# Optimization experiments

Hardware: AMD Instinct MI355X
Metric: run time of the kernel (lower is better)

## Reference

```python
import jax, jax.numpy as jnp
import numpy as np

DMODEL = 1024
DHIDDEN = 1024
N_HEAD = 16
HEAD_DIM = DHIDDEN // N_HEAD
B, S = 4, 2048


def setup_inputs() -> dict:
    key = jax.random.key(0)
    ks = jax.random.split(key, 10)
    sc = 1.0 / np.sqrt(DMODEL)
    return {
        "x": jax.random.normal(ks[0], (B, S, DMODEL), dtype=jnp.float32),
        "Wq": jax.random.normal(ks[1], (DMODEL, DHIDDEN), dtype=jnp.float32) * sc,
        "bq": jnp.zeros((DHIDDEN,), dtype=jnp.float32),
        "Wk": jax.random.normal(ks[2], (DMODEL, DHIDDEN), dtype=jnp.float32) * sc,
        "bk": jnp.zeros((DHIDDEN,), dtype=jnp.float32),
        "Wv": jax.random.normal(ks[3], (DMODEL, DHIDDEN), dtype=jnp.float32) * sc,
        "bv": jnp.zeros((DHIDDEN,), dtype=jnp.float32),
        "Wo": jax.random.normal(ks[4], (DHIDDEN, DMODEL), dtype=jnp.float32) * sc,
        "bo": jnp.zeros((DMODEL,), dtype=jnp.float32),
        "ln_gamma": jnp.ones((DMODEL,), dtype=jnp.float32),
        "ln_beta": jnp.zeros((DMODEL,), dtype=jnp.float32),
    }


def _layernorm(x, gamma, beta, eps=1e-5):
    mu = jnp.mean(x, axis=-1, keepdims=True)
    var = jnp.var(x, axis=-1, keepdims=True)
    return (x - mu) * jax.lax.rsqrt(var + eps) * gamma + beta


def reference(x, Wq, bq, Wk, bk, Wv, bv, Wo, bo, ln_gamma, ln_beta):
    b, s, _ = x.shape
    h = _layernorm(x, ln_gamma, ln_beta)           # [B,S,D]
    q = h @ Wq + bq                                 # [B,S,Dh]
    k = h @ Wk + bk
    v = h @ Wv + bv
    # [B,H,S,hd]
    q = q.reshape(b, s, N_HEAD, HEAD_DIM).transpose(0, 2, 1, 3)
    k = k.reshape(b, s, N_HEAD, HEAD_DIM).transpose(0, 2, 1, 3)
    v = v.reshape(b, s, N_HEAD, HEAD_DIM).transpose(0, 2, 1, 3)
    scores = jnp.einsum("bhqd,bhkd->bhqk", q, k) / np.sqrt(HEAD_DIM)
    causal = jnp.tril(jnp.ones((s, s), dtype=bool))  # [S,S]
    scores = jnp.where(causal, scores, jnp.finfo(scores.dtype).min)
    attn = jax.nn.softmax(scores, axis=-1)           # [B,H,S,S]
    out = jnp.einsum("bhqk,bhkd->bhqd", attn, v)     # [B,H,S,hd]
    out = out.transpose(0, 2, 1, 3).reshape(b, s, DHIDDEN)
    return out @ Wo + bo
```

## Files before the change

kernel.cpp:

```cpp
#include <hip/hip_runtime.h>


typedef short short8 __attribute__((ext_vector_type(8)));
typedef float floatx4 __attribute__((ext_vector_type(4)));
typedef unsigned short ushort4v __attribute__((ext_vector_type(4)));
typedef unsigned int uint2v __attribute__((ext_vector_type(2)));

#define MFMA16(a, b, c) __builtin_amdgcn_mfma_f32_16x16x32_bf16((a), (b), (c), 0, 0, 0)

__device__ __forceinline__ unsigned short f2bf(float f) {
  unsigned int u = __float_as_uint(f);
  u += 0x7FFFu + ((u >> 16) & 1u);
  return (unsigned short)(u >> 16);
}

#if defined(__has_builtin)
#if __has_builtin(__builtin_amdgcn_cvt_pk_bf16_f32)
#define HAVE_PK_BF16 1
#endif
#if __has_builtin(__builtin_amdgcn_exp2f)
#define EXP2(x) __builtin_amdgcn_exp2f(x)
#endif
#if __has_builtin(__builtin_amdgcn_rcpf)
#define RCP(x) __builtin_amdgcn_rcpf(x)
#endif
#endif
#ifndef EXP2
#define EXP2(x) exp2f(x)
#endif
#ifndef RCP
#define RCP(x) (1.0f / (x))
#endif

__device__ __forceinline__ unsigned int pk_bf16(float a, float b) {
#ifdef HAVE_PK_BF16
  typedef __bf16 bf16x2_t __attribute__((ext_vector_type(2)));
  union { bf16x2_t v; unsigned int u; } cvt;
  cvt.v = __builtin_amdgcn_cvt_pk_bf16_f32(a, b);
  return cvt.u;
#else
  return (unsigned int)f2bf(a) | ((unsigned int)f2bf(b) << 16);
#endif
}

__device__ __forceinline__ void async_lds16(const void* g, void* l) {
  __builtin_amdgcn_global_load_lds(
      (const __attribute__((address_space(1))) void*)g,
      (__attribute__((address_space(3))) void*)l, 16, 0, 0);
}

__global__ __launch_bounds__(256) void prep_kernel(
    const float* __restrict__ wq, const float* __restrict__ wk,
    const float* __restrict__ wv, const float* __restrict__ wo,
    unsigned short* __restrict__ wqkvT, unsigned short* __restrict__ woT,
    const float* __restrict__ x, const float* __restrict__ gamma,
    const float* __restrict__ beta, unsigned short* __restrict__ h) {
  __shared__ float t[64][65];
  __shared__ float sm[4], qm[4];
  const int id = (int)blockIdx.x;
  const int tid = threadIdx.x;
  if (id < 1024) {
    const int mz = id >> 8, rem = id & 255;
    const int n0 = (rem & 15) * 64, k0 = (rem >> 4) * 64;
    const int r = tid >> 6, c = tid & 63;
    const float* src = (mz == 0) ? wq : (mz == 1) ? wk : (mz == 2) ? wv : wo;
    unsigned short* dst = (mz == 3) ? woT : (wqkvT + (size_t)mz * 1024 * 1024);
#pragma unroll
    for (int i = r; i < 64; i += 4) t[i][c] = src[(size_t)(k0 + i) * 1024 + n0 + c];
    __syncthreads();
#pragma unroll
    for (int i = r; i < 64; i += 4)
      dst[(size_t)(n0 + i) * 1024 + k0 + c] = f2bf(t[c][i]);
    return;
  }
  const int row = id - 1024;
  const float4 xv = ((const float4*)(x + (size_t)row * 1024))[tid];
  float s = xv.x + xv.y + xv.z + xv.w;
  float q = xv.x * xv.x + xv.y * xv.y + xv.z * xv.z + xv.w * xv.w;
#pragma unroll
  for (int off = 32; off > 0; off >>= 1) {
    s += __shfl_xor(s, off, 64);
    q += __shfl_xor(q, off, 64);
  }
  const int wave = tid >> 6, lane = tid & 63;
  if (lane == 0) { sm[wave] = s; qm[wave] = q; }
  __syncthreads();
  s = sm[0] + sm[1] + sm[2] + sm[3];
  q = qm[0] + qm[1] + qm[2] + qm[3];
  const float mean = s * (1.0f / 1024.0f);
  const float var = q * (1.0f / 1024.0f) - mean * mean;
  const float rstd = rsqrtf(var + 1e-5f);
  const float4 g = ((const float4*)gamma)[tid];
  const float4 bb = ((const float4*)beta)[tid];
  ushort4v o;
  o.x = f2bf((xv.x - mean) * rstd * g.x + bb.x);
  o.y = f2bf((xv.y - mean) * rstd * g.y + bb.y);
  o.z = f2bf((xv.z - mean) * rstd * g.z + bb.z);
  o.w = f2bf((xv.w - mean) * rstd * g.w + bb.w);
  ((ushort4v*)(h + (size_t)row * 1024))[tid] = o;
}

#define GEMM128_MAIN(A_, Bt_, m0_, n0_)                                         \
  __shared__ __align__(16) unsigned short lA[128 * 64];                         \
  __shared__ __align__(16) unsigned short lB[128 * 64];                         \
  const int tid = threadIdx.x;                                                  \
  const int wave = tid >> 6, lane = tid & 63, quad = lane >> 4, l15 = lane & 15;\
  const int wm = wave >> 1, wn = wave & 1;                                      \
  const int m0 = (m0_), n0 = (n0_);                                             \
  const int srow = tid >> 3, schunk = tid & 7;                                  \
  const int swz = l15 & 7;                                                      \
  floatx4 acc[4][4];                                                            \
  _Pragma("unroll") for (int i = 0; i < 4; i++)                                 \
  _Pragma("unroll") for (int j = 0; j < 4; j++)                                 \
      acc[i][j] = (floatx4){0.f, 0.f, 0.f, 0.f};                                \
  for (int kt = 0; kt < 16; kt++) {                                             \
    const int k0 = kt * 64;                                                     \
    __syncthreads();                                                            \
    _Pragma("unroll") for (int j = 0; j < 4; j++) {                             \
      const int row_ = j * 32 + srow;                                           \
      const int gch_ = schunk ^ (row_ & 7);                                     \
      async_lds16(A_ + (size_t)(m0 + row_) * 1024 + k0 + gch_ * 8,              \
                  (char*)lA + j * 4096 + wave * 1024);                          \
      async_lds16(Bt_ + (size_t)(n0 + row_) * 1024 + k0 + gch_ * 8,             \
                  (char*)lB + j * 4096 + wave * 1024);                          \
    }                                                                           \
    __syncthreads();                                                            \
    _Pragma("unroll") for (int kk = 0; kk < 2; kk++) {                          \
      const int ch = (kk * 4 + quad) ^ swz;                                     \
      short8 af[4], bf[4];                                                      \
      _Pragma("unroll") for (int i = 0; i < 4; i++) {                           \
        af[i] = *(const short8*)(lA + (wm * 64 + i * 16 + l15) * 64 + ch * 8);  \
        bf[i] = *(const short8*)(lB + (wn * 64 + i * 16 + l15) * 64 + ch * 8);  \
      }                                                                         \
      _Pragma("unroll") for (int mt = 0; mt < 4; mt++)                          \
      _Pragma("unroll") for (int nt = 0; nt < 4; nt++)                          \
          acc[mt][nt] = MFMA16(af[mt], bf[nt], acc[mt][nt]);                    \
    }                                                                           \
  }

__global__ __launch_bounds__(512, 2) void gemm_qkv(
    const unsigned short* __restrict__ A, const unsigned short* __restrict__ Bt,
    const float* __restrict__ bq, const float* __restrict__ bk,
    const float* __restrict__ bv, unsigned short* __restrict__ qo,
    unsigned short* __restrict__ ko, unsigned short* __restrict__ vT) {
  __shared__ __align__(16) unsigned short lA[2][2][128 * 64];
  __shared__ __align__(16) unsigned short lB[2][2][128 * 64];
  const int tid = threadIdx.x;
  const int wave = tid >> 6, lane = tid & 63, quad = lane >> 4, l15 = lane & 15;
  const int wm = wave >> 2, wn = wave & 3;
  const int id = (int)blockIdx.x;
  const int xcd = id & 7, rr = id >> 3;
  const int m0 = (xcd * 4 + (rr & 3)) * 256;
  const int n0 = (rr >> 2) * 256;

  const int srow8 = tid >> 3, chunk8 = tid & 7;
  const int gch = chunk8 ^ (srow8 & 7);
  const int wave1024 = wave * 1024;
  const int swz = l15 & 7;
  const int ch0 = quad ^ swz, ch1 = (4 + quad) ^ swz;

  const unsigned short* pA0 = A + (size_t)(m0 + srow8) * 1024 + gch * 8;
  const unsigned short* pA1 = pA0 + (size_t)128 * 1024;
  const unsigned short* pB0 = Bt + (size_t)(n0 + srow8) * 1024 + gch * 8;
  const unsigned short* pB1 = pB0 + (size_t)128 * 1024;

  const unsigned short* rdA[2] = {&lA[0][wm][0] + l15 * 64,
                                  &lA[1][wm][0] + l15 * 64};
  const unsigned short* rdB[2] = {&lB[0][wn >> 1][0] + ((wn & 1) * 64 + l15) * 64,
                                  &lB[1][wn >> 1][0] + ((wn & 1) * 64 + l15) * 64};

  floatx4 acc[8][4];
#pragma unroll
  for (int i = 0; i < 8; i++)
#pragma unroll
    for (int j = 0; j < 4; j++) acc[i][j] = (floatx4){0.f, 0.f, 0.f, 0.f};

  short8 bF[4][2], aQ0[2][2], aQ1[2][2], aQ2[2][2], aQ3[2][2];

#define STG(p_, k0_, dst_)                                                     \
  {                                                                            \
    _Pragma("unroll") for (int j_ = 0; j_ < 2; j_++)                           \
        async_lds16((p_) + (size_t)j_ * 65536 + (k0_),                         \
                    (char*)(dst_) + j_ * 8192 + wave1024);                     \
  }
#define LDB(buf_)                                                              \
  _Pragma("unroll") for (int n_ = 0; n_ < 4; n_++) {                           \
    bF[n_][0] = *(const short8*)(rdB[buf_] + n_ * 1024 + ch0 * 8);             \
    bF[n_][1] = *(const short8*)(rdB[buf_] + n_ * 1024 + ch1 * 8);             \
  }
#define LDA(dst_, mb_, buf_)                                                   \
  _Pragma("unroll") for (int mm_ = 0; mm_ < 2; mm_++) {                        \
    dst_[mm_][0] = *(const short8*)(rdA[buf_] + ((mb_) + mm_) * 1024 + ch0 * 8);\
    dst_[mm_][1] = *(const short8*)(rdA[buf_] + ((mb_) + mm_) * 1024 + ch1 * 8);\
  }
#define MFQ(af_, q_)                                                           \
  __builtin_amdgcn_s_setprio(1);                                              \
  _Pragma("unroll") for (int mm_ = 0; mm_ < 2; mm_++)                          \
  _Pragma("unroll") for (int n_ = 0; n_ < 4; n_++) {                           \
    acc[(q_)*2 + mm_][n_] = MFMA16(af_[mm_][0], bF[n_][0], acc[(q_)*2 + mm_][n_]); \
    acc[(q_)*2 + mm_][n_] = MFMA16(af_[mm_][1], bF[n_][1], acc[(q_)*2 + mm_][n_]); \
  }                                                                            \
  __builtin_amdgcn_s_setprio(0);
#define BAR()                                                                  \
  {                                                                            \
    asm volatile("" ::: "memory");                                             \
    __builtin_amdgcn_s_barrier();                                              \
    asm volatile("" ::: "memory");                                             \
  }
#define WAITV(n_)                                                              \
  {                                                                            \
    asm volatile("s_waitcnt vmcnt(" #n_ ")" ::: "memory");                     \
    __builtin_amdgcn_sched_barrier(0);                                         \
  }

  STG(pB0, 0, &lB[0][0][0]);
  STG(pB1, 0, &lB[0][1][0]);
  STG(pA0, 0, &lA[0][0][0]);
  STG(pA1, 0, &lA[0][1][0]);
  STG(pB0, 64, &lB[1][0][0]);
  STG(pB1, 64, &lB[1][1][0]);
  STG(pA0, 64, &lA[1][0][0]);
  WAITV(6);
  BAR();

  for (int i = 0; i < 7; i++) {
    const int kA = (2 * i + 1) * 64;
    const int kB = kA + 64;
    const int kC = kB + 64;
    LDB(0); LDA(aQ0, 0, 0);
    STG(pA1, kA, &lA[1][1][0]);
    BAR(); MFQ(aQ0, 0); BAR();
    LDA(aQ1, 2, 0); LDA(aQ2, 4, 0);
    STG(pB0, kB, &lB[0][0][0]);
    BAR(); MFQ(aQ1, 1); BAR();
    LDA(aQ3, 6, 0);
    STG(pB1, kB, &lB[0][1][0]);
    BAR(); MFQ(aQ2, 2); BAR();
    STG(pA0, kB, &lA[0][0][0]);
    WAITV(6);
    BAR(); MFQ(aQ3, 3); BAR();
    LDB(1); LDA(aQ0, 0, 1);
    STG(pA1, kB, &lA[0][1][0]);
    BAR(); MFQ(aQ0, 0); BAR();
    LDA(aQ1, 2, 1); LDA(aQ2, 4, 1);
    STG(pB0, kC, &lB[1][0][0]);
    BAR(); MFQ(aQ1, 1); BAR();
    LDA(aQ3, 6, 1);
    STG(pB1, kC, &lB[1][1][0]);
    BAR(); MFQ(aQ2, 2); BAR();
    STG(pA0, kC, &lA[1][0][0]);
    WAITV(6);
    BAR(); MFQ(aQ3, 3); BAR();
  }
  LDB(0); LDA(aQ0, 0, 0);
  STG(pA1, 15 * 64, &lA[1][1][0]);
  BAR(); MFQ(aQ0, 0); BAR();
  LDA(aQ1, 2, 0); LDA(aQ2, 4, 0);
  BAR(); MFQ(aQ1, 1); BAR();
  LDA(aQ3, 6, 0);
  BAR(); MFQ(aQ2, 2); BAR();
  WAITV(0);
  BAR(); MFQ(aQ3, 3); BAR();
  LDB(1); LDA(aQ0, 0, 1);
  MFQ(aQ0, 0);
  LDA(aQ1, 2, 1); LDA(aQ2, 4, 1);
  MFQ(aQ1, 1);
  LDA(aQ3, 6, 1);
  MFQ(aQ2, 2);
  MFQ(aQ3, 3);

  const int sel = n0 >> 10;
  const float* bias = (sel == 0) ? bq : (sel == 1) ? bk : bv;
  const float oscale = (sel == 0) ? 0.18033688011112042f : 1.0f;
#pragma unroll
  for (int nt = 0; nt < 4; nt++) {
    const int n = n0 + wn * 64 + nt * 16 + l15;
    const int nn = n & 1023;
    const float bia = bias[nn];
    const int hidx = nn >> 6, d = nn & 63;
#pragma unroll
    for (int mt = 0; mt < 8; mt++) {
      const int mb = m0 + wm * 128 + mt * 16 + quad * 4;
      const int b = mb >> 11, sdx = mb & 2047;
      if (sel == 2) {
        ushort4v pk;
#pragma unroll
        for (int r = 0; r < 4; r++) pk[r] = f2bf(acc[mt][nt][r] + bia);
        *(ushort4v*)(vT + ((size_t)(b * 16 + hidx) * 64 + d) * 2048 + sdx) = pk;
      } else {
        unsigned short* dst =
            ((sel == 0) ? qo : ko) + ((size_t)(b * 16 + hidx) * 2048 + sdx) * 64 + d;
#pragma unroll
        for (int r = 0; r < 4; r++)
          dst[(size_t)r * 64] = f2bf((acc[mt][nt][r] + bia) * oscale);
      }
    }
  }
#undef STG
#undef LDB
#undef LDA
#undef MFQ
#undef BAR
#undef WAITV
}

__global__ __launch_bounds__(256) void gemm_out(
    const unsigned short* __restrict__ A, const unsigned short* __restrict__ Bt,
    const float* __restrict__ bo, float* __restrict__ out) {
  const int id = (int)blockIdx.x;
  GEMM128_MAIN(A, Bt, (id >> 3) * 128, (id & 7) * 128)
#pragma unroll
  for (int nt = 0; nt < 4; nt++) {
    const int n = n0 + wn * 64 + nt * 16 + l15;
    const float bia = bo[n];
#pragma unroll
    for (int mt = 0; mt < 4; mt++) {
      const int m = m0 + wm * 64 + mt * 16 + quad * 4;
#pragma unroll
      for (int r = 0; r < 4; r++) out[(size_t)(m + r) * 1024 + n] = acc[mt][nt][r] + bia;
    }
  }
}

__global__ __launch_bounds__(256, 4) void attn_kernel(
    const unsigned short* __restrict__ q, const unsigned short* __restrict__ k,
    const unsigned short* __restrict__ vT, unsigned short* __restrict__ ao) {
  __shared__ __align__(16) unsigned short lK[2][64 * 64];
  __shared__ __align__(16) unsigned short lV[2][64 * 64];
  __shared__ __align__(16) unsigned short lP[4][16 * 64];
  const int tid = threadIdx.x;
  const int wave = tid >> 6, lane = tid & 63, quad = lane >> 4, l15 = lane & 15;
  const int id = (int)blockIdx.x;
  const int bh = (id & 7) * 8 + ((id >> 3) & 7);
  const int qx = id >> 6;
  const int b = bh >> 4, hh = bh & 15;
  const int qtA = 31 - qx, qtB = qx;
  const int q0wA = qtA * 64 + wave * 16, q0wB = qtB * 64 + wave * 16;
  const int ntiles = qtA + 1;

  const unsigned short* qb = q + (size_t)bh * 2048 * 64;
  const unsigned short* kb = k + (size_t)bh * 2048 * 64;
  const unsigned short* vb = vT + (size_t)bh * 64 * 2048;
  unsigned short* pw = &lP[wave][0];

  const int srow = tid >> 3, schunk = tid & 7;

  const short8 ones8 = {0x3F80, 0x3F80, 0x3F80, 0x3F80,
                        0x3F80, 0x3F80, 0x3F80, 0x3F80};

  const int sw = l15 & 7;
  const int ph0 = (0 * 4 + quad) ^ sw, ph1 = (1 * 4 + quad) ^ sw;

#define STAGE_TILE(src_, rstride_, cbase_, dst_)                                 \
  _Pragma("unroll") for (int j = 0; j < 2; j++) {                                \
    const int row_ = j * 32 + srow;                                              \
    const int gch_ = schunk ^ (row_ & 7);                                        \
    async_lds16(src_ + (size_t)row_ * (rstride_) + (cbase_) + gch_ * 8,          \
                (char*)(dst_) + j * 4096 + wave * 1024);                         \
  }

  short8 qfA[2], qfB[2];
#pragma unroll
  for (int hf = 0; hf < 2; hf++) {
    qfA[hf] = *(const short8*)(qb + (size_t)(q0wA + l15) * 64 + hf * 32 + quad * 8);
    qfB[hf] = *(const short8*)(qb + (size_t)(q0wB + l15) * 64 + hf * 32 + quad * 8);
  }

  floatx4 oA[4], oB[4];
#pragma unroll
  for (int nt = 0; nt < 4; nt++) {
    oA[nt] = (floatx4){0.f, 0.f, 0.f, 0.f};
    oB[nt] = (floatx4){0.f, 0.f, 0.f, 0.f};
  }
  floatx4 laccA = {0.f, 0.f, 0.f, 0.f}, laccB = {0.f, 0.f, 0.f, 0.f};

  STAGE_TILE(kb, 64, 0, &lK[0][0])
  STAGE_TILE(vb, 2048, 0, &lV[0][0])
  int kbase = 0;
  for (int t = 0; t < ntiles; t++, kbase += 64) {
    __syncthreads();
    if (t + 1 < ntiles) {
      const int nb = (t + 1) & 1;
      STAGE_TILE(kb, 64, (size_t)(kbase + 64) * 64, &lK[nb][0])
      STAGE_TILE(vb, 2048, (size_t)(kbase + 64), &lV[nb][0])
    }
    const unsigned short* lKc = &lK[t & 1][0];
    const unsigned short* lVc = &lV[t & 1][0];
    const bool dual = (t <= qtB);

    floatx4 scA[4], scB[4];
#pragma unroll
    for (int nt = 0; nt < 4; nt++) {
      scA[nt] = (floatx4){0.f, 0.f, 0.f, 0.f};
      scB[nt] = (floatx4){0.f, 0.f, 0.f, 0.f};
      const short8 kf0 = *(const short8*)(lKc + (nt * 16 + l15) * 64 + ph0 * 8);
      const short8 kf1 = *(const short8*)(lKc + (nt * 16 + l15) * 64 + ph1 * 8);
      scA[nt] = MFMA16(kf0, qfA[0], scA[nt]);
      scA[nt] = MFMA16(kf1, qfA[1], scA[nt]);
      if (dual) {
        scB[nt] = MFMA16(kf0, qfB[0], scB[nt]);
        scB[nt] = MFMA16(kf1, qfB[1], scB[nt]);
      }
    }

    {
      const bool needmask = (kbase + 63 > q0wA);
      const int qg = q0wA + l15;
#pragma unroll
      for (int nt = 0; nt < 4; nt++) {
        float p0 = EXP2(scA[nt][0]), p1 = EXP2(scA[nt][1]);
        float p2 = EXP2(scA[nt][2]), p3 = EXP2(scA[nt][3]);
        if (needmask) {
          const int kk = kbase + nt * 16 + quad * 4;
          if (kk + 0 > qg) p0 = 0.f;
          if (kk + 1 > qg) p1 = 0.f;
          if (kk + 2 > qg) p2 = 0.f;
          if (kk + 3 > qg) p3 = 0.f;
        }
        uint2v pk2;
        pk2.x = pk_bf16(p0, p1);
        pk2.y = pk_bf16(p2, p3);
        const int phys = (nt * 2 + (quad >> 1)) ^ sw;
        *(uint2v*)(pw + l15 * 64 + phys * 8 + (quad & 1) * 4) = pk2;
      }
    }
    asm volatile("s_waitcnt lgkmcnt(0)" ::: "memory");
    short8 pfA0 = *(const short8*)(pw + l15 * 64 + ph0 * 8);
    short8 pfA1 = *(const short8*)(pw + l15 * 64 + ph1 * 8);

    short8 pfB0, pfB1;
    if (dual) {
      const bool needmask = (kbase + 63 > q0wB);
      const int qg = q0wB + l15;
#pragma unroll
      for (int nt = 0; nt < 4; nt++) {
        float p0 = EXP2(scB[nt][0]), p1 = EXP2(scB[nt][1]);
        float p2 = EXP2(scB[nt][2]), p3 = EXP2(scB[nt][3]);
        if (needmask) {
          const int kk = kbase + nt * 16 + quad * 4;
          if (kk + 0 > qg) p0 = 0.f;
          if (kk + 1 > qg) p1 = 0.f;
          if (kk + 2 > qg) p2 = 0.f;
          if (kk + 3 > qg) p3 = 0.f;
        }
        uint2v pk2;
        pk2.x = pk_bf16(p0, p1);
        pk2.y = pk_bf16(p2, p3);
        const int phys = (nt * 2 + (quad >> 1)) ^ sw;
        *(uint2v*)(pw + l15 * 64 + phys * 8 + (quad & 1) * 4) = pk2;
      }
      asm volatile("s_waitcnt lgkmcnt(0)" ::: "memory");
      pfB0 = *(const short8*)(pw + l15 * 64 + ph0 * 8);
      pfB1 = *(const short8*)(pw + l15 * 64 + ph1 * 8);
    }

#pragma unroll
    for (int hf = 0; hf < 2; hf++) {
      const short8 pfA = hf ? pfA1 : pfA0;
      laccA = MFMA16(ones8, pfA, laccA);
      if (dual) laccB = MFMA16(ones8, hf ? pfB1 : pfB0, laccB);
      const int ph = hf ? ph1 : ph0;
#pragma unroll
      for (int nt = 0; nt < 4; nt++) {
        const short8 vf = *(const short8*)(lVc + (nt * 16 + l15) * 64 + ph * 8);
        oA[nt] = MFMA16(vf, pfA, oA[nt]);
        if (dual) oB[nt] = MFMA16(vf, hf ? pfB1 : pfB0, oB[nt]);
      }
    }
  }

  {
    const float linv = RCP(laccA[0]);
    unsigned short* dst = ao + ((size_t)b * 2048 + q0wA + l15) * 1024 + hh * 64;
#pragma unroll
    for (int nt = 0; nt < 4; nt++) {
      uint2v pk2;
      pk2.x = pk_bf16(oA[nt][0] * linv, oA[nt][1] * linv);
      pk2.y = pk_bf16(oA[nt][2] * linv, oA[nt][3] * linv);
      *(uint2v*)(dst + nt * 16 + quad * 4) = pk2;
    }
  }
  {
    const float linv = RCP(laccB[0]);
    unsigned short* dst = ao + ((size_t)b * 2048 + q0wB + l15) * 1024 + hh * 64;
#pragma unroll
    for (int nt = 0; nt < 4; nt++) {
      uint2v pk2;
      pk2.x = pk_bf16(oB[nt][0] * linv, oB[nt][1] * linv);
      pk2.y = pk_bf16(oB[nt][2] * linv, oB[nt][3] * linv);
      *(uint2v*)(dst + nt * 16 + quad * 4) = pk2;
    }
  }
#undef STAGE_TILE
}

extern "C" void kernel_launch(void* const* d_in, const int* in_sizes, int n_in,
                              void* d_out, int out_size, void* d_ws, size_t ws_size,
                              hipStream_t stream) {
  const float* x = (const float*)d_in[0];
  const float* Wq = (const float*)d_in[1];
  const float* bq = (const float*)d_in[2];
  const float* Wk = (const float*)d_in[3];
  const float* bk = (const float*)d_in[4];
  const float* Wv = (const float*)d_in[5];
  const float* bv = (const float*)d_in[6];
  const float* Wo = (const float*)d_in[7];
  const float* bo = (const float*)d_in[8];
  const float* gamma = (const float*)d_in[9];
  const float* beta = (const float*)d_in[10];
  float* out = (float*)d_out;

  char* ws = (char*)d_ws;
  unsigned short* wqkvT = (unsigned short*)(ws + 0);
  unsigned short* woT   = (unsigned short*)(ws + 6291456);
  unsigned short* h     = (unsigned short*)(ws + 8388608);
  unsigned short* qb    = (unsigned short*)(ws + 25165824);
  unsigned short* kb    = (unsigned short*)(ws + 41943040);
  unsigned short* vT    = (unsigned short*)(ws + 58720256);
  unsigned short* ao    = (unsigned short*)(ws + 75497472);

  hipLaunchKernelGGL(prep_kernel, dim3(9216), dim3(256), 0, stream,
                     Wq, Wk, Wv, Wo, wqkvT, woT, x, gamma, beta, h);
  hipLaunchKernelGGL(gemm_qkv, dim3(384), dim3(512), 0, stream,
                     h, wqkvT, bq, bk, bv, qb, kb, vT);
  hipLaunchKernelGGL(attn_kernel, dim3(1024), dim3(256), 0, stream, qb, kb, vT, ao);
  hipLaunchKernelGGL(gemm_out, dim3(512), dim3(256), 0, stream, ao, woT, bo, out);
}
```

Baseline: 276.5 us.

## Replace hand-pipelined 256x256 QKV GEMM with 128x128 tiles and LDS-staged epilogue

Result: faster. 262.1 us (-5.2%).

```diff
diff --git a/kernel.cpp b/kernel.cpp
--- a/kernel.cpp
+++ b/kernel.cpp
@@ -101,8 +101,9 @@
 }
 
 #define GEMM128_MAIN(A_, Bt_, m0_, n0_)                                         \
-  __shared__ __align__(16) unsigned short lA[128 * 64];                         \
-  __shared__ __align__(16) unsigned short lB[128 * 64];                         \
+  __shared__ __align__(16) unsigned short lAB[2][128 * 64];                     \
+  unsigned short* const lA = &lAB[0][0];                                        \
+  unsigned short* const lB = &lAB[1][0];                                        \
   const int tid = threadIdx.x;                                                  \
   const int wave = tid >> 6, lane = tid & 63, quad = lane >> 4, l15 = lane & 15;\
   const int wm = wave >> 1, wn = wave & 1;                                      \
@@ -138,170 +139,75 @@
     }                                                                           \
   }
 
-__global__ __launch_bounds__(512, 2) void gemm_qkv(
+__global__ __launch_bounds__(256) void gemm_qkv(
     const unsigned short* __restrict__ A, const unsigned short* __restrict__ Bt,
     const float* __restrict__ bq, const float* __restrict__ bk,
     const float* __restrict__ bv, unsigned short* __restrict__ qo,
     unsigned short* __restrict__ ko, unsigned short* __restrict__ vT) {
-  __shared__ __align__(16) unsigned short lA[2][2][128 * 64];
-  __shared__ __align__(16) unsigned short lB[2][2][128 * 64];
-  const int tid = threadIdx.x;
-  const int wave = tid >> 6, lane = tid & 63, quad = lane >> 4, l15 = lane & 15;
-  const int wm = wave >> 2, wn = wave & 3;
   const int id = (int)blockIdx.x;
   const int xcd = id & 7, rr = id >> 3;
-  const int m0 = (xcd * 4 + (rr & 3)) * 256;
-  const int n0 = (rr >> 2) * 256;
-
-  const int srow8 = tid >> 3, chunk8 = tid & 7;
-  const int gch = chunk8 ^ (srow8 & 7);
-  const int wave1024 = wave * 1024;
-  const int swz = l15 & 7;
-  const int ch0 = quad ^ swz, ch1 = (4 + quad) ^ swz;
-
-  const unsigned short* pA0 = A + (size_t)(m0 + srow8) * 1024 + gch * 8;
-  const unsigned short* pA1 = pA0 + (size_t)128 * 1024;
-  const unsigned short* pB0 = Bt + (size_t)(n0 + srow8) * 1024 + gch * 8;
-  const unsigned short* pB1 = pB0 + (size_t)128 * 1024;
-
-  const unsigned short* rdA[2] = {&lA[0][wm][0] + l15 * 64,
-                                  &lA[1][wm][0] + l15 * 64};
-  const unsigned short* rdB[2] = {&lB[0][wn >> 1][0] + ((wn & 1) * 64 + l15) * 64,
-                                  &lB[1][wn >> 1][0] + ((wn & 1) * 64 + l15) * 64};
-
-  floatx4 acc[8][4];
-#pragma unroll
-  for (int i = 0; i < 8; i++)
-#pragma unroll
-    for (int j = 0; j < 4; j++) acc[i][j] = (floatx4){0.f, 0.f, 0.f, 0.f};
-
-  short8 bF[4][2], aQ0[2][2], aQ1[2][2], aQ2[2][2], aQ3[2][2];
-
-#define STG(p_, k0_, dst_)                                                     \
-  {                                                                            \
-    _Pragma("unroll") for (int j_ = 0; j_ < 2; j_++)                           \
-        async_lds16((p_) + (size_t)j_ * 65536 + (k0_),                         \
-                    (char*)(dst_) + j_ * 8192 + wave1024);                     \
-  }
-#define LDB(buf_)                                                              \
-  _Pragma("unroll") for (int n_ = 0; n_ < 4; n_++) {                           \
-    bF[n_][0] = *(const short8*)(rdB[buf_] + n_ * 1024 + ch0 * 8);             \
-    bF[n_][1] = *(const short8*)(rdB[buf_] + n_ * 1024 + ch1 * 8);             \
-  }
-#define LDA(dst_, mb_, buf_)                                                   \
-  _Pragma("unroll") for (int mm_ = 0; mm_ < 2; mm_++) {                        \
-    dst_[mm_][0] = *(const short8*)(rdA[buf_] + ((mb_) + mm_) * 1024 + ch0 * 8);\
-    dst_[mm_][1] = *(const short8*)(rdA[buf_] + ((mb_) + mm_) * 1024 + ch1 * 8);\
-  }
-#define MFQ(af_, q_)                                                           \
-  __builtin_amdgcn_s_setprio(1);                                              \
-  _Pragma("unroll") for (int mm_ = 0; mm_ < 2; mm_++)                          \
-  _Pragma("unroll") for (int n_ = 0; n_ < 4; n_++) {                           \
-    acc[(q_)*2 + mm_][n_] = MFMA16(af_[mm_][0], bF[n_][0], acc[(q_)*2 + mm_][n_]); \
-    acc[(q_)*2 + mm_][n_] = MFMA16(af_[mm_][1], bF[n_][1], acc[(q_)*2 + mm_][n_]); \
-  }                                                                            \
-  __builtin_amdgcn_s_setprio(0);
-#define BAR()                                                                  \
-  {                                                                            \
-    asm volatile("" ::: "memory");                                             \
-    __builtin_amdgcn_s_barrier();                                              \
-    asm volatile("" ::: "memory");                                             \
-  }
-#define WAITV(n_)                                                              \
-  {                                                                            \
-    asm volatile("s_waitcnt vmcnt(" #n_ ")" ::: "memory");                     \
-    __builtin_amdgcn_sched_barrier(0);                                         \
-  }
-
-  STG(pB0, 0, &lB[0][0][0]);
-  STG(pB1, 0, &lB[0][1][0]);
-  STG(pA0, 0, &lA[0][0][0]);
-  STG(pA1, 0, &lA[0][1][0]);
-  STG(pB0, 64, &lB[1][0][0]);
-  STG(pB1, 64, &lB[1][1][0]);
-  STG(pA0, 64, &lA[1][0][0]);
-  WAITV(6);
-  BAR();
-
-  for (int i = 0; i < 7; i++) {
-    const int kA = (2 * i + 1) * 64;
-    const int kB = kA + 64;
-    const int kC = kB + 64;
-    LDB(0); LDA(aQ0, 0, 0);
-    STG(pA1, kA, &lA[1][1][0]);
-    BAR(); MFQ(aQ0, 0); BAR();
-    LDA(aQ1, 2, 0); LDA(aQ2, 4, 0);
-    STG(pB0, kB, &lB[0][0][0]);
-    BAR(); MFQ(aQ1, 1); BAR();
-    LDA(aQ3, 6, 0);
-    STG(pB1, kB, &lB[0][1][0]);
-    BAR(); MFQ(aQ2, 2); BAR();
-    STG(pA0, kB, &lA[0][0][0]);
-    WAITV(6);
-    BAR(); MFQ(aQ3, 3); BAR();
-    LDB(1); LDA(aQ0, 0, 1);
-    STG(pA1, kB, &lA[0][1][0]);
-    BAR(); MFQ(aQ0, 0); BAR();
-    LDA(aQ1, 2, 1); LDA(aQ2, 4, 1);
-    STG(pB0, kC, &lB[1][0][0]);
-    BAR(); MFQ(aQ1, 1); BAR();
-    LDA(aQ3, 6, 1);
-    STG(pB1, kC, &lB[1][1][0]);
-    BAR(); MFQ(aQ2, 2); BAR();
-    STG(pA0, kC, &lA[1][0][0]);
-    WAITV(6);
-    BAR(); MFQ(aQ3, 3); BAR();
-  }
-  LDB(0); LDA(aQ0, 0, 0);
-  STG(pA1, 15 * 64, &lA[1][1][0]);
-  BAR(); MFQ(aQ0, 0); BAR();
-  LDA(aQ1, 2, 0); LDA(aQ2, 4, 0);
-  BAR(); MFQ(aQ1, 1); BAR();
-  LDA(aQ3, 6, 0);
-  BAR(); MFQ(aQ2, 2); BAR();
-  WAITV(0);
-  BAR(); MFQ(aQ3, 3); BAR();
-  LDB(1); LDA(aQ0, 0, 1);
-  MFQ(aQ0, 0);
-  LDA(aQ1, 2, 1); LDA(aQ2, 4, 1);
-  MFQ(aQ1, 1);
-  LDA(aQ3, 6, 1);
-  MFQ(aQ2, 2);
-  MFQ(aQ3, 3);
-
+  GEMM128_MAIN(A, Bt, (rr / 3) * 128, (xcd * 3 + (rr % 3)) * 128)
   const int sel = n0 >> 10;
   const float* bias = (sel == 0) ? bq : (sel == 1) ? bk : bv;
   const float oscale = (sel == 0) ? 0.18033688011112042f : 1.0f;
-#pragma unroll
-  for (int nt = 0; nt < 4; nt++) {
-    const int n = n0 + wn * 64 + nt * 16 + l15;
-    const int nn = n & 1023;
-    const float bia = bias[nn];
-    const int hidx = nn >> 6, d = nn & 63;
-#pragma unroll
-    for (int mt = 0; mt < 8; mt++) {
-      const int mb = m0 + wm * 128 + mt * 16 + quad * 4;
-      const int b = mb >> 11, sdx = mb & 2047;
-      if (sel == 2) {
+  unsigned short* const st = &lAB[0][0];
+  const int b16 = (m0 >> 11) * 16;
+  const int h0 = (n0 & 1023) >> 6;
+  const int ms = m0 & 2047;
+  __syncthreads();
+  if (sel == 2) {
+#pragma unroll
+    for (int nt = 0; nt < 4; nt++) {
+      const int nl = wn * 64 + nt * 16 + l15;
+      const float bia = bias[(n0 + nl) & 1023];
+      const int x = (nl & 15) << 1;
+#pragma unroll
+      for (int mt = 0; mt < 4; mt++) {
+        const int chunk = wm * 16 + mt * 4 + quad;
         ushort4v pk;
 #pragma unroll
         for (int r = 0; r < 4; r++) pk[r] = f2bf(acc[mt][nt][r] + bia);
-        *(ushort4v*)(vT + ((size_t)(b * 16 + hidx) * 64 + d) * 2048 + sdx) = pk;
-      } else {
-        unsigned short* dst =
-            ((sel == 0) ? qo : ko) + ((size_t)(b * 16 + hidx) * 2048 + sdx) * 64 + d;
-#pragma unroll
-        for (int r = 0; r < 4; r++)
-          dst[(size_t)r * 64] = f2bf((acc[mt][nt][r] + bia) * oscale);
-      }
-    }
-  }
-#undef STG
-#undef LDB
-#undef LDA
-#undef MFQ
-#undef BAR
-#undef WAITV
+        *(ushort4v*)((char*)st + nl * 256 + ((chunk ^ x) << 3)) = pk;
+      }
+    }
+    __syncthreads();
+#pragma unroll
+    for (int p = 0; p < 8; p++) {
+      const int nl = p * 16 + (tid >> 4);
+      const int j2 = tid & 15;
+      const short8 vv =
+          *(const short8*)((char*)st + nl * 256 + ((j2 ^ (nl & 15)) << 4));
+      *(short8*)(vT + ((size_t)(b16 + h0 + (nl >> 6)) * 64 + (nl & 63)) * 2048 +
+                 ms + j2 * 8) = vv;
+    }
+  } else {
+#pragma unroll
+    for (int nt = 0; nt < 4; nt++) {
+      const int nl = wn * 64 + nt * 16 + l15;
+      const float bia = bias[(n0 + nl) & 1023];
+      const int chunk = nl >> 3, nin = nl & 7;
+#pragma unroll
+      for (int mt = 0; mt < 4; mt++) {
+#pragma unroll
+        for (int r = 0; r < 4; r++) {
+          const int ml = wm * 64 + mt * 16 + quad * 4 + r;
+          *(unsigned short*)((char*)st + ml * 256 + ((chunk ^ (ml & 7)) << 4) +
+                             nin * 2) = f2bf((acc[mt][nt][r] + bia) * oscale);
+        }
+      }
+    }
+    __syncthreads();
+    unsigned short* const dq = (sel == 0) ? qo : ko;
+#pragma unroll
+    for (int p = 0; p < 8; p++) {
+      const int ml = p * 16 + (tid >> 4);
+      const int j = tid & 15;
+      const short8 vv =
+          *(const short8*)((char*)st + ml * 256 + ((j ^ (ml & 7)) << 4));
+      *(short8*)(dq + ((size_t)(b16 + h0 + (j >> 3)) * 2048 + (ms + ml)) * 64 +
+                 (j & 7) * 8) = vv;
+    }
+  }
 }
 
 __global__ __launch_bounds__(256) void gemm_out(
@@ -389,6 +295,7 @@
     const bool dual = (t <= qtB);
 
     floatx4 scA[4], scB[4];
+    __builtin_amdgcn_s_setprio(1);
 #pragma unroll
     for (int nt = 0; nt < 4; nt++) {
       scA[nt] = (floatx4){0.f, 0.f, 0.f, 0.f};
@@ -402,6 +309,7 @@
         scB[nt] = MFMA16(kf1, qfB[1], scB[nt]);
       }
     }
+    __builtin_amdgcn_s_setprio(0);
 
     {
       const bool needmask = (kbase + 63 > q0wA);
@@ -454,6 +362,7 @@
       pfB1 = *(const short8*)(pw + l15 * 64 + ph1 * 8);
     }
 
+    __builtin_amdgcn_s_setprio(1);
 #pragma unroll
     for (int hf = 0; hf < 2; hf++) {
       const short8 pfA = hf ? pfA1 : pfA0;
@@ -467,6 +376,7 @@
         if (dual) oB[nt] = MFMA16(vf, hf ? pfB1 : pfB0, oB[nt]);
       }
     }
+    __builtin_amdgcn_s_setprio(0);
   }
 
   {
@@ -521,7 +431,7 @@
 
   hipLaunchKernelGGL(prep_kernel, dim3(9216), dim3(256), 0, stream,
                      Wq, Wk, Wv, Wo, wqkvT, woT, x, gamma, beta, h);
-  hipLaunchKernelGGL(gemm_qkv, dim3(384), dim3(512), 0, stream,
+  hipLaunchKernelGGL(gemm_qkv, dim3(1536), dim3(256), 0, stream,
                      h, wqkvT, bq, bk, bv, qb, kb, vT);
   hipLaunchKernelGGL(attn_kernel, dim3(1024), dim3(256), 0, stream, qb, kb, vT, ao);
   hipLaunchKernelGGL(gemm_out, dim3(512), dim3(256), 0, stream, ao, woT, bo, out);
```
